# Kernel optimization log

Hardware: AMD Instinct MI355X
Metric: run time of the kernel (lower is better)

## Reference

```python
import jax, jax.numpy as jnp
import numpy as np

B, P, N = 1024, 100, 101
EMB, H, DK = 128, 8, 16
SQRT_EMB = 11.313708498984761
CLIP = 10.0


def setup_inputs() -> dict:
    key = jax.random.key(0)
    ks = jax.random.split(key, 12)
    inp = {
        "encoded_last_node": jax.random.normal(ks[0], (B, P, EMB), jnp.float32),
        "load": jax.random.uniform(ks[1], (B, P), jnp.float32),
        "time": jax.random.uniform(ks[2], (B, P), jnp.float32),
        "length": jax.random.uniform(ks[3], (B, P), jnp.float32),
        "route_open": jax.random.uniform(ks[4], (B, P), jnp.float32),
        "ninf_mask": jnp.zeros((B, P, N), jnp.float32),
        "encoded_nodes": jax.random.normal(ks[5], (B, N, EMB), jnp.float32),
        # weights stored [in, out]
        "Wq": jax.random.normal(ks[6], (EMB + 4, H * DK), jnp.float32) * 0.05,
        "Wk": jax.random.normal(ks[7], (EMB, H * DK), jnp.float32) * 0.05,
        "Wv": jax.random.normal(ks[8], (EMB, H * DK), jnp.float32) * 0.05,
        "Wc": jax.random.normal(ks[9], (H * DK, EMB), jnp.float32) * 0.05,
        "bc": jax.random.normal(ks[10], (EMB,), jnp.float32) * 0.05,
    }
    return inp


def _heads(x):
    # [B, n, H*DK] -> [B, H, n, DK]
    b, n, _ = x.shape
    return x.reshape(b, n, H, DK).transpose(0, 2, 1, 3)


def reference(encoded_last_node, load, time, length, route_open, ninf_mask,
              encoded_nodes, Wq, Wk, Wv, Wc, bc):
    # set_kv
    k = _heads(encoded_nodes @ Wk)            # [B,H,N,DK]
    v = _heads(encoded_nodes @ Wv)            # [B,H,N,DK]
    # forward
    input_cat = jnp.concatenate(
        [encoded_last_node, load[:, :, None], time[:, :, None],
         length[:, :, None], route_open[:, :, None]], axis=2)  # [B,P,EMB+4]
    q = _heads(input_cat @ Wq)                # [B,H,P,DK]
    score = jnp.einsum('bhpd,bhnd->bhpn', q, k) / jnp.sqrt(jnp.float32(DK))
    score = score + ninf_mask[:, None, :, :]
    weights = jax.nn.softmax(score, axis=3)
    out = jnp.einsum('bhpn,bhnd->bhpd', weights, v)
    out_concat = out.transpose(0, 2, 1, 3).reshape(out.shape[0], out.shape[2], H * DK)
    mh = out_concat @ Wc + bc                 # [B,P,EMB]
    score2 = jnp.einsum('bpe,bne->bpn', mh, encoded_nodes) / SQRT_EMB
    score2 = CLIP * jnp.tanh(score2) + ninf_mask
    probs = jax.nn.softmax(score2, axis=2)
    return probs
```

## Files before the change

kernel.cpp:

```cpp
#include <hip/hip_runtime.h>
#include <stdint.h>

#define B_    1024
#define P_    100
#define N_    101
#define EMB_  128
#define H_    8
#define DK_   16

#define ROWS  112
#define KSTR  136

typedef uint16_t bf16;
typedef __attribute__((ext_vector_type(8))) short short8;
typedef __attribute__((ext_vector_type(4))) float float4v;

#define L2E 1.4426950408889634f

#if __has_builtin(__builtin_amdgcn_exp2f)
#define EXP2(x) __builtin_amdgcn_exp2f(x)
#else
#define EXP2(x) exp2f(x)
#endif
#if __has_builtin(__builtin_amdgcn_rcpf)
#define RCP(x) __builtin_amdgcn_rcpf(x)
#else
#define RCP(x) (1.0f / (x))
#endif

__device__ __forceinline__ float b2f(bf16 u) {
    union { uint32_t i; float f; } c; c.i = ((uint32_t)u) << 16; return c.f;
}
__device__ __forceinline__ bf16 f2b(float f) {
    union { float f; uint32_t i; } c; c.f = f;
    return (bf16)((c.i + 0x8000u) >> 16);
}
__device__ __forceinline__ uint32_t pk2(float a, float b) {
    union { float f; uint32_t i; } ca, cb; ca.f = a; cb.f = b;
    return __builtin_amdgcn_perm(cb.i + 0x8000u, ca.i + 0x8000u, 0x07060302u);
}

__device__ __forceinline__ void stage_m(const float* __restrict__ src, int nrows,
                                        bf16* __restrict__ dst, int tid) {
    for (int i = tid; i < ROWS * 32; i += 1024) {
        int r = i >> 5, c = (i & 31) << 2;
        uint32_t p0 = 0, p1 = 0;
        if (r < nrows) {
            float4 v = *(const float4*)(src + (size_t)r * EMB_ + c);
            p0 = pk2(v.x, v.y); p1 = pk2(v.z, v.w);
        }
        uint32_t* d = (uint32_t*)(dst + r * KSTR + c);
        d[0] = p0; d[1] = p1;
    }
}

__global__ __launch_bounds__(256)
void prep_wT(const float* __restrict__ Wq, const float* __restrict__ Wk,
             const float* __restrict__ Wv, const float* __restrict__ Wc,
             bf16* __restrict__ ws) {
    int idx = blockIdx.x * 256 + threadIdx.x;
    int w = idx >> 14, rem = idx & 16383;
    int k = rem >> 7, o = rem & 127;
    const float* W = (w == 0) ? Wk : (w == 1) ? Wv : (w == 2) ? Wq : Wc;
    ws[((size_t)w << 14) + o * 128 + k] = f2b(W[(size_t)k * 128 + o]);
}

__global__ __launch_bounds__(1024, 4)
void vrp_kernel(const float* __restrict__ eln,
                const float* __restrict__ load_,
                const float* __restrict__ time_,
                const float* __restrict__ len_,
                const float* __restrict__ open_,
                const float* __restrict__ mask_,
                const float* __restrict__ enc_,
                const float* __restrict__ Wq,
                const float* __restrict__ bc,
                const bf16* __restrict__ wsWT,
                float* __restrict__ out)
{
    const int b    = blockIdx.x;
    const int tid  = threadIdx.x;
    const int wave = tid >> 6;
    const int lane = tid & 63;
    const int lr = lane & 15, lq = lane >> 4, lk = lq << 3;

    __shared__ bf16 smem[78336];
    __shared__ float sS4[ROWS * 4];
    __shared__ float sWq4[4 * EMB_];
    bf16* const R1 = smem;
    bf16* const R2 = smem + 15232;
    bf16* const R3 = smem + 30464;
    bf16* const R4 = smem + 47872;
    bf16* const R5 = smem + 63104;

    const bf16* WkT = wsWT;
    const bf16* WvT = wsWT + 16384;
    const bf16* WqT = wsWT + 32768;
    const bf16* WcT = wsWT + 49152;

    const float* encB  = enc_  + (size_t)b * N_ * EMB_;
    const float* elnB  = eln   + (size_t)b * P_ * EMB_;
    const float* maskB = mask_ + (size_t)b * P_ * N_;
    float*       outB  = out   + (size_t)b * P_ * N_;

    stage_m(encB, N_, R1, tid);
    stage_m(elnB, P_, R5, tid);
    if (tid < 512) {
        int d = tid >> 2, c = 112 + ((tid & 3) << 2);
        uint32_t* z = (uint32_t*)(R3 + d * KSTR + c);
        z[0] = 0; z[1] = 0;
    }
    if (tid < ROWS * 4) {
        int r = tid >> 2, j = tid & 3;
        float v = 0.f;
        if (r < P_) {
            const float* s4 = (j == 0) ? load_ : (j == 1) ? time_
                             : (j == 2) ? len_ : open_;
            v = s4[(size_t)b * P_ + r];
        }
        sS4[r * 4 + j] = v;
    }
    if (tid < 512) {
        int j = tid >> 7, c = tid & 127;
        sWq4[j * EMB_ + c] = Wq[(size_t)(EMB_ + j) * EMB_ + c];
    }
    __syncthreads();

    {
        const int col = 16 * (wave & 7) + lr;
        const int mt0 = (wave >> 3) ? 4 : 0;
        const int mt1 = (wave >> 3) ? 7 : 4;
        short8 bk[4], bv[4], bq[4];
        {
            const bf16* rk = WkT + (size_t)col * 128 + lk;
            const bf16* rv = WvT + (size_t)col * 128 + lk;
            const bf16* rq = WqT + (size_t)col * 128 + lk;
            #pragma unroll
            for (int s = 0; s < 4; ++s) {
                bk[s] = *(const short8*)(rk + s * 32);
                bv[s] = *(const short8*)(rv + s * 32);
                bq[s] = *(const short8*)(rq + s * 32);
            }
        }
        float w0 = sWq4[col], w1 = sWq4[EMB_ + col];
        float w2 = sWq4[2 * EMB_ + col], w3 = sWq4[3 * EMB_ + col];
        for (int mt = mt0; mt < mt1; ++mt) {
            short8 a[4];
            #pragma unroll
            for (int s = 0; s < 4; ++s)
                a[s] = *(const short8*)(R1 + (mt * 16 + lr) * KSTR + s * 32 + lk);
            float4v ck = {0.f, 0.f, 0.f, 0.f}, cv = {0.f, 0.f, 0.f, 0.f};
            #pragma unroll
            for (int s = 0; s < 4; ++s) {
                ck = __builtin_amdgcn_mfma_f32_16x16x32_bf16(a[s], bk[s], ck, 0, 0, 0);
                cv = __builtin_amdgcn_mfma_f32_16x16x32_bf16(a[s], bv[s], cv, 0, 0, 0);
            }
            int n0 = mt * 16 + (lq << 2);
            #pragma unroll
            for (int r = 0; r < 4; ++r)
                R2[(n0 + r) * KSTR + col] = f2b(ck[r]);
            uint32_t* d = (uint32_t*)(R3 + col * KSTR + n0);
            d[0] = pk2(cv[0], cv[1]);
            d[1] = pk2(cv[2], cv[3]);
            short8 aq[4];
            #pragma unroll
            for (int s = 0; s < 4; ++s)
                aq[s] = *(const short8*)(R5 + (mt * 16 + lr) * KSTR + s * 32 + lk);
            float4v cq = {0.f, 0.f, 0.f, 0.f};
            #pragma unroll
            for (int s = 0; s < 4; ++s)
                cq = __builtin_amdgcn_mfma_f32_16x16x32_bf16(aq[s], bq[s], cq, 0, 0, 0);
            int row0 = mt * 16 + (lq << 2);
            #pragma unroll
            for (int r = 0; r < 4; ++r) {
                const float* s4 = sS4 + (row0 + r) * 4;
                float acc = cq[r] + s4[0] * w0 + s4[1] * w1 + s4[2] * w2 + s4[3] * w3;
                R4[(row0 + r) * KSTR + col] = f2b(acc * (0.25f * L2E));
            }
        }
    }
    __syncthreads();

    const int hg = (wave >= 7) ? 1 : 0;
    const int pt = wave - hg * 7;
    float4v o4[4];
    if (wave < 14) {
        bf16* Pbuf = hg ? R5 : R1;
        {
            uint32_t* z = (uint32_t*)(Pbuf + (pt * 16 + lr) * KSTR + 112 + (lq << 2));
            z[0] = 0; z[1] = 0;
        }
        float msk2[7][4];
        {
            const int p = pt * 16 + lr;
            const bool pvalid = (p < P_);
            const float* mrow = maskB + (size_t)(pvalid ? p : 0) * N_;
            #pragma unroll
            for (int nt = 0; nt < 7; ++nt) {
                int nb = nt * 16 + (lq << 2);
                #pragma unroll
                for (int r = 0; r < 4; ++r) {
                    int n = nb + r;
                    float v;
                    if (n >= N_) v = -3.0e38f;
                    else v = pvalid ? mrow[n] * L2E : 0.f;
                    msk2[nt][r] = v;
                }
            }
        }
        #pragma unroll
        for (int hh = 0; hh < 4; ++hh) {
            int h  = hg * 4 + hh;
            int k0 = (h >> 1) << 5;
            short8 bq = *(const short8*)(R4 + (pt * 16 + lr) * KSTR + k0 + lk);
            if ((lq >> 1) != (h & 1)) bq = (short8){0,0,0,0,0,0,0,0};
            float sc[7][4];
            __builtin_amdgcn_s_setprio(1);
            #pragma unroll
            for (int nt = 0; nt < 7; ++nt) {
                short8 ak = *(const short8*)(R2 + (nt * 16 + lr) * KSTR + k0 + lk);
                float4v cc = {msk2[nt][0], msk2[nt][1], msk2[nt][2], msk2[nt][3]};
                cc = __builtin_amdgcn_mfma_f32_16x16x32_bf16(ak, bq, cc, 0, 0, 0);
                #pragma unroll
                for (int r = 0; r < 4; ++r) sc[nt][r] = cc[r];
            }
            __builtin_amdgcn_s_setprio(0);
            float mm[7];
            #pragma unroll
            for (int nt = 0; nt < 7; ++nt)
                mm[nt] = fmaxf(fmaxf(sc[nt][0], sc[nt][1]),
                               fmaxf(sc[nt][2], sc[nt][3]));
            float m = fmaxf(fmaxf(fmaxf(mm[0], mm[1]), fmaxf(mm[2], mm[3])),
                            fmaxf(fmaxf(mm[4], mm[5]), mm[6]));
            m = fmaxf(m, __shfl_xor(m, 16));
            m = fmaxf(m, __shfl_xor(m, 32));
            float s0 = 0.f, s1 = 0.f, s2 = 0.f, s3 = 0.f;
            #pragma unroll
            for (int nt = 0; nt < 7; ++nt) {
                float e0 = EXP2(sc[nt][0] - m); sc[nt][0] = e0; s0 += e0;
                float e1 = EXP2(sc[nt][1] - m); sc[nt][1] = e1; s1 += e1;
                float e2 = EXP2(sc[nt][2] - m); sc[nt][2] = e2; s2 += e2;
                float e3 = EXP2(sc[nt][3] - m); sc[nt][3] = e3; s3 += e3;
            }
            float su = (s0 + s1) + (s2 + s3);
            su += __shfl_xor(su, 16);
            su += __shfl_xor(su, 32);
            float inv = RCP(su);
            float invp[4];
            #pragma unroll
            for (int r = 0; r < 4; ++r) invp[r] = __shfl(inv, (lq << 2) + r);
            #pragma unroll
            for (int nt = 0; nt < 7; ++nt) {
                uint32_t* d = (uint32_t*)(Pbuf + (pt * 16 + lr) * KSTR
                                          + nt * 16 + (lq << 2));
                d[0] = pk2(sc[nt][0], sc[nt][1]);
                d[1] = pk2(sc[nt][2], sc[nt][3]);
            }
            float4v o = {0.f, 0.f, 0.f, 0.f};
            __builtin_amdgcn_s_setprio(1);
            #pragma unroll
            for (int ks = 0; ks < 128; ks += 32) {
                short8 a2 = *(const short8*)(Pbuf + (pt * 16 + lr) * KSTR + ks + lk);
                short8 b2 = *(const short8*)(R3 + (h * 16 + lr) * KSTR + ks + lk);
                o = __builtin_amdgcn_mfma_f32_16x16x32_bf16(a2, b2, o, 0, 0, 0);
            }
            __builtin_amdgcn_s_setprio(0);
            #pragma unroll
            for (int r = 0; r < 4; ++r) o[r] *= invp[r];
            o4[hh] = o;
        }
    }
    float fmsk[7][4];
    if (wave < 7) {
        #pragma unroll
        for (int nt = 0; nt < 7; ++nt) {
            int n = nt * 16 + lr;
            #pragma unroll
            for (int r = 0; r < 4; ++r) {
                int p = wave * 16 + (lq << 2) + r;
                float v;
                if (n >= N_) v = -3.0e38f;
                else if (p < P_) v = maskB[(size_t)p * N_ + n] * L2E;
                else v = 0.f;
                fmsk[nt][r] = v;
            }
        }
    }
    __syncthreads();

    if (wave < 14) {
        #pragma unroll
        for (int hh = 0; hh < 4; ++hh) {
            int h = hg * 4 + hh;
            #pragma unroll
            for (int r = 0; r < 4; ++r)
                R4[(pt * 16 + (lq << 2) + r) * KSTR + h * 16 + lr] = f2b(o4[hh][r]);
        }
    }
    stage_m(encB, N_, R2, tid);
    __syncthreads();

    {
        const int col = 16 * (wave & 7) + lr;
        const int mt0 = (wave >> 3) ? 4 : 0;
        const int mt1 = (wave >> 3) ? 7 : 4;
        short8 bw[4];
        {
            const bf16* rc = WcT + (size_t)col * 128 + lk;
            #pragma unroll
            for (int s = 0; s < 4; ++s) bw[s] = *(const short8*)(rc + s * 32);
        }
        float bcv = bc[col];
        for (int mt = mt0; mt < mt1; ++mt) {
            short8 a[4];
            #pragma unroll
            for (int s = 0; s < 4; ++s)
                a[s] = *(const short8*)(R4 + (mt * 16 + lr) * KSTR + s * 32 + lk);
            float4v c = {0.f, 0.f, 0.f, 0.f};
            #pragma unroll
            for (int s = 0; s < 4; ++s)
                c = __builtin_amdgcn_mfma_f32_16x16x32_bf16(a[s], bw[s], c, 0, 0, 0);
            int row0 = mt * 16 + (lq << 2);
            #pragma unroll
            for (int r = 0; r < 4; ++r) {
                float m = c[r] + bcv;
                bf16 hb = f2b(m);
                R1[(row0 + r) * KSTR + col] = hb;
                R5[(row0 + r) * KSTR + col] = f2b(m - b2f(hb));
            }
        }
    }
    __syncthreads();

    if (wave < 7) {
        const int pt2 = wave;
        short8 ahi[4], alo[4];
        #pragma unroll
        for (int s = 0; s < 4; ++s) {
            ahi[s] = *(const short8*)(R1 + (pt2 * 16 + lr) * KSTR + s * 32 + lk);
            alo[s] = *(const short8*)(R5 + (pt2 * 16 + lr) * KSTR + s * 32 + lk);
        }
        float sc[7][4];
        #pragma unroll
        for (int nt = 0; nt < 7; ++nt) {
            float4v cc = {0.f, 0.f, 0.f, 0.f};
            #pragma unroll
            for (int s = 0; s < 4; ++s) {
                short8 bb = *(const short8*)(R2 + (nt * 16 + lr) * KSTR + s * 32 + lk);
                cc = __builtin_amdgcn_mfma_f32_16x16x32_bf16(ahi[s], bb, cc, 0, 0, 0);
                cc = __builtin_amdgcn_mfma_f32_16x16x32_bf16(alo[s], bb, cc, 0, 0, 0);
            }
            #pragma unroll
            for (int r = 0; r < 4; ++r) {
                float y = EXP2(cc[r] * (0.08838834764831845f * 2.0f * L2E));
                float t = fmaf(-2.0f, RCP(y + 1.0f), 1.0f);
                sc[nt][r] = fmaf(10.0f * L2E, t, fmsk[nt][r]);
            }
        }
        #pragma unroll
        for (int r = 0; r < 4; ++r) {
            float m = sc[0][r];
            #pragma unroll
            for (int nt = 1; nt < 7; ++nt) m = fmaxf(m, sc[nt][r]);
            #pragma unroll
            for (int d = 1; d < 16; d <<= 1) m = fmaxf(m, __shfl_xor(m, d));
            float su = 0.f;
            #pragma unroll
            for (int nt = 0; nt < 7; ++nt) {
                float e = EXP2(sc[nt][r] - m); sc[nt][r] = e; su += e;
            }
            #pragma unroll
            for (int d = 1; d < 16; d <<= 1) su += __shfl_xor(su, d);
            float inv = RCP(su);
            int p = pt2 * 16 + (lq << 2) + r;
            if (p < P_) {
                #pragma unroll
                for (int nt = 0; nt < 7; ++nt) {
                    int n = nt * 16 + lr;
                    if (n < N_) outB[(size_t)p * N_ + n] = sc[nt][r] * inv;
                }
            }
        }
    }
}

extern "C" void kernel_launch(void* const* d_in, const int* in_sizes, int n_in,
                              void* d_out, int out_size, void* d_ws, size_t ws_size,
                              hipStream_t stream) {
    const float* eln   = (const float*)d_in[0];
    const float* load_ = (const float*)d_in[1];
    const float* time_ = (const float*)d_in[2];
    const float* len_  = (const float*)d_in[3];
    const float* open_ = (const float*)d_in[4];
    const float* mask_ = (const float*)d_in[5];
    const float* enc_  = (const float*)d_in[6];
    const float* Wq    = (const float*)d_in[7];
    const float* Wk    = (const float*)d_in[8];
    const float* Wv    = (const float*)d_in[9];
    const float* Wc    = (const float*)d_in[10];
    const float* bc    = (const float*)d_in[11];
    float* out = (float*)d_out;
    bf16* wsWT = (bf16*)d_ws;

    prep_wT<<<dim3(256), dim3(256), 0, stream>>>(Wq, Wk, Wv, Wc, wsWT);
    vrp_kernel<<<dim3(B_), dim3(1024), 0, stream>>>(
        eln, load_, time_, len_, open_, mask_, enc_, Wq, bc, wsWT, out);
}
```

Measured before the change: 308.1 us.

## Transpose final score MFMA to reuse mask registers and vectorize mask/output access

Swaps the A/B operands of the final score MFMA so each lane holds a row of p with n along registers. This lets the second softmax reuse the attention mask registers and write output rows with 16-byte stores instead of scalar strided stores. The mask is loaded with vector loads, the second mask load is dropped, the softmax normalization is folded into the probabilities before the PV MFMA, and the setprio hints are removed. The F4 casts on rows of 101 floats are not 16-byte aligned for most rows, which risks misaligned vector access penalties.

```diff
diff --git a/kernel.cpp b/kernel.cpp
--- a/kernel.cpp
+++ b/kernel.cpp
@@ -14,6 +14,8 @@
 typedef uint16_t bf16;
 typedef __attribute__((ext_vector_type(8))) short short8;
 typedef __attribute__((ext_vector_type(4))) float float4v;
+
+struct F4 { float x, y, z, w; };
 
 #define L2E 1.4426950408889634f
 
@@ -183,6 +185,7 @@
 
     const int hg = (wave >= 7) ? 1 : 0;
     const int pt = wave - hg * 7;
+    float msk2[7][4];
     float4v o4[4];
     if (wave < 14) {
         bf16* Pbuf = hg ? R5 : R1;
@@ -190,22 +193,31 @@
             uint32_t* z = (uint32_t*)(Pbuf + (pt * 16 + lr) * KSTR + 112 + (lq << 2));
             z[0] = 0; z[1] = 0;
         }
-        float msk2[7][4];
         {
             const int p = pt * 16 + lr;
             const bool pvalid = (p < P_);
             const float* mrow = maskB + (size_t)(pvalid ? p : 0) * N_;
             #pragma unroll
-            for (int nt = 0; nt < 7; ++nt) {
+            for (int nt = 0; nt < 6; ++nt) {
                 int nb = nt * 16 + (lq << 2);
-                #pragma unroll
-                for (int r = 0; r < 4; ++r) {
-                    int n = nb + r;
-                    float v;
-                    if (n >= N_) v = -3.0e38f;
-                    else v = pvalid ? mrow[n] * L2E : 0.f;
-                    msk2[nt][r] = v;
-                }
+                F4 mv = *(const F4*)(mrow + nb);
+                msk2[nt][0] = pvalid ? mv.x * L2E : 0.f;
+                msk2[nt][1] = pvalid ? mv.y * L2E : 0.f;
+                msk2[nt][2] = pvalid ? mv.z * L2E : 0.f;
+                msk2[nt][3] = pvalid ? mv.w * L2E : 0.f;
+            }
+            if (lq == 0) {
+                F4 mv = *(const F4*)(mrow + 96);
+                msk2[6][0] = pvalid ? mv.x * L2E : 0.f;
+                msk2[6][1] = pvalid ? mv.y * L2E : 0.f;
+                msk2[6][2] = pvalid ? mv.z * L2E : 0.f;
+                msk2[6][3] = pvalid ? mv.w * L2E : 0.f;
+            } else if (lq == 1) {
+                msk2[6][0] = pvalid ? mrow[100] * L2E : 0.f;
+                msk2[6][1] = -3.0e38f; msk2[6][2] = -3.0e38f; msk2[6][3] = -3.0e38f;
+            } else {
+                msk2[6][0] = -3.0e38f; msk2[6][1] = -3.0e38f;
+                msk2[6][2] = -3.0e38f; msk2[6][3] = -3.0e38f;
             }
         }
         #pragma unroll
@@ -215,7 +227,6 @@
             short8 bq = *(const short8*)(R4 + (pt * 16 + lr) * KSTR + k0 + lk);
             if ((lq >> 1) != (h & 1)) bq = (short8){0,0,0,0,0,0,0,0};
             float sc[7][4];
-            __builtin_amdgcn_s_setprio(1);
             #pragma unroll
             for (int nt = 0; nt < 7; ++nt) {
                 short8 ak = *(const short8*)(R2 + (nt * 16 + lr) * KSTR + k0 + lk);
@@ -224,7 +235,6 @@
                 #pragma unroll
                 for (int r = 0; r < 4; ++r) sc[nt][r] = cc[r];
             }
-            __builtin_amdgcn_s_setprio(0);
             float mm[7];
             #pragma unroll
             for (int nt = 0; nt < 7; ++nt)
@@ -246,44 +256,21 @@
             su += __shfl_xor(su, 16);
             su += __shfl_xor(su, 32);
             float inv = RCP(su);
-            float invp[4];
-            #pragma unroll
-            for (int r = 0; r < 4; ++r) invp[r] = __shfl(inv, (lq << 2) + r);
             #pragma unroll
             for (int nt = 0; nt < 7; ++nt) {
                 uint32_t* d = (uint32_t*)(Pbuf + (pt * 16 + lr) * KSTR
                                           + nt * 16 + (lq << 2));
-                d[0] = pk2(sc[nt][0], sc[nt][1]);
-                d[1] = pk2(sc[nt][2], sc[nt][3]);
+                d[0] = pk2(sc[nt][0] * inv, sc[nt][1] * inv);
+                d[1] = pk2(sc[nt][2] * inv, sc[nt][3] * inv);
             }
             float4v o = {0.f, 0.f, 0.f, 0.f};
-            __builtin_amdgcn_s_setprio(1);
             #pragma unroll
             for (int ks = 0; ks < 128; ks += 32) {
                 short8 a2 = *(const short8*)(Pbuf + (pt * 16 + lr) * KSTR + ks + lk);
                 short8 b2 = *(const short8*)(R3 + (h * 16 + lr) * KSTR + ks + lk);
                 o = __builtin_amdgcn_mfma_f32_16x16x32_bf16(a2, b2, o, 0, 0, 0);
             }
-            __builtin_amdgcn_s_setprio(0);
-            #pragma unroll
-            for (int r = 0; r < 4; ++r) o[r] *= invp[r];
             o4[hh] = o;
-        }
-    }
-    float fmsk[7][4];
-    if (wave < 7) {
-        #pragma unroll
-        for (int nt = 0; nt < 7; ++nt) {
-            int n = nt * 16 + lr;
-            #pragma unroll
-            for (int r = 0; r < 4; ++r) {
-                int p = wave * 16 + (lq << 2) + r;
-                float v;
-                if (n >= N_) v = -3.0e38f;
-                else if (p < P_) v = maskB[(size_t)p * N_ + n] * L2E;
-                else v = 0.f;
-                fmsk[nt][r] = v;
-            }
         }
     }
     __syncthreads();
@@ -334,11 +321,11 @@
 
     if (wave < 7) {
         const int pt2 = wave;
-        short8 ahi[4], alo[4];
+        short8 bhi[4], blo[4];
         #pragma unroll
         for (int s = 0; s < 4; ++s) {
-            ahi[s] = *(const short8*)(R1 + (pt2 * 16 + lr) * KSTR + s * 32 + lk);
-            alo[s] = *(const short8*)(R5 + (pt2 * 16 + lr) * KSTR + s * 32 + lk);
+            bhi[s] = *(const short8*)(R1 + (pt2 * 16 + lr) * KSTR + s * 32 + lk);
+            blo[s] = *(const short8*)(R5 + (pt2 * 16 + lr) * KSTR + s * 32 + lk);
         }
         float sc[7][4];
         #pragma unroll
@@ -346,39 +333,53 @@
             float4v cc = {0.f, 0.f, 0.f, 0.f};
             #pragma unroll
             for (int s = 0; s < 4; ++s) {
-                short8 bb = *(const short8*)(R2 + (nt * 16 + lr) * KSTR + s * 32 + lk);
-                cc = __builtin_amdgcn_mfma_f32_16x16x32_bf16(ahi[s], bb, cc, 0, 0, 0);
-                cc = __builtin_amdgcn_mfma_f32_16x16x32_bf16(alo[s], bb, cc, 0, 0, 0);
+                short8 ae = *(const short8*)(R2 + (nt * 16 + lr) * KSTR + s * 32 + lk);
+                cc = __builtin_amdgcn_mfma_f32_16x16x32_bf16(ae, bhi[s], cc, 0, 0, 0);
+                cc = __builtin_amdgcn_mfma_f32_16x16x32_bf16(ae, blo[s], cc, 0, 0, 0);
             }
             #pragma unroll
             for (int r = 0; r < 4; ++r) {
                 float y = EXP2(cc[r] * (0.08838834764831845f * 2.0f * L2E));
                 float t = fmaf(-2.0f, RCP(y + 1.0f), 1.0f);
-                sc[nt][r] = fmaf(10.0f * L2E, t, fmsk[nt][r]);
-            }
-        }
-        #pragma unroll
-        for (int r = 0; r < 4; ++r) {
-            float m = sc[0][r];
-            #pragma unroll
-            for (int nt = 1; nt < 7; ++nt) m = fmaxf(m, sc[nt][r]);
-            #pragma unroll
-            for (int d = 1; d < 16; d <<= 1) m = fmaxf(m, __shfl_xor(m, d));
-            float su = 0.f;
-            #pragma unroll
-            for (int nt = 0; nt < 7; ++nt) {
-                float e = EXP2(sc[nt][r] - m); sc[nt][r] = e; su += e;
-            }
-            #pragma unroll
-            for (int d = 1; d < 16; d <<= 1) su += __shfl_xor(su, d);
-            float inv = RCP(su);
-            int p = pt2 * 16 + (lq << 2) + r;
-            if (p < P_) {
-                #pragma unroll
-                for (int nt = 0; nt < 7; ++nt) {
-                    int n = nt * 16 + lr;
-                    if (n < N_) outB[(size_t)p * N_ + n] = sc[nt][r] * inv;
-                }
+                sc[nt][r] = fmaf(10.0f * L2E, t, msk2[nt][r]);
+            }
+        }
+        float mm[7];
+        #pragma unroll
+        for (int nt = 0; nt < 7; ++nt)
+            mm[nt] = fmaxf(fmaxf(sc[nt][0], sc[nt][1]),
+                           fmaxf(sc[nt][2], sc[nt][3]));
+        float m = fmaxf(fmaxf(fmaxf(mm[0], mm[1]), fmaxf(mm[2], mm[3])),
+                        fmaxf(fmaxf(mm[4], mm[5]), mm[6]));
+        m = fmaxf(m, __shfl_xor(m, 16));
+        m = fmaxf(m, __shfl_xor(m, 32));
+        float s0 = 0.f, s1 = 0.f, s2 = 0.f, s3 = 0.f;
+        #pragma unroll
+        for (int nt = 0; nt < 7; ++nt) {
+            float e0 = EXP2(sc[nt][0] - m); sc[nt][0] = e0; s0 += e0;
+            float e1 = EXP2(sc[nt][1] - m); sc[nt][1] = e1; s1 += e1;
+            float e2 = EXP2(sc[nt][2] - m); sc[nt][2] = e2; s2 += e2;
+            float e3 = EXP2(sc[nt][3] - m); sc[nt][3] = e3; s3 += e3;
+        }
+        float su = (s0 + s1) + (s2 + s3);
+        su += __shfl_xor(su, 16);
+        su += __shfl_xor(su, 32);
+        float inv = RCP(su);
+        const int p = pt2 * 16 + lr;
+        if (p < P_) {
+            float* orow = outB + (size_t)p * N_;
+            #pragma unroll
+            for (int nt = 0; nt < 6; ++nt) {
+                F4 ov = { sc[nt][0] * inv, sc[nt][1] * inv,
+                          sc[nt][2] * inv, sc[nt][3] * inv };
+                *(F4*)(orow + nt * 16 + (lq << 2)) = ov;
+            }
+            if (lq == 0) {
+                F4 ov = { sc[6][0] * inv, sc[6][1] * inv,
+                          sc[6][2] * inv, sc[6][3] * inv };
+                *(F4*)(orow + 96) = ov;
+            } else if (lq == 1) {
+                orow[100] = sc[6][0] * inv;
             }
         }
     }
```

Result: faster. 274.0 us (-11.0%).
